# Kernel tuning notes

Hardware: AMD Instinct MI355X
Metric: run time of the kernel (lower is better)

Reference implementation:

```python
import jax, jax.numpy as jnp
import numpy as np

EMBED_DIM = 1024
NUM_HEADS = 16
HEAD_DIM = EMBED_DIM // NUM_HEADS
SCALING = HEAD_DIM ** -0.5
TGT_LEN, BSZ = 2048, 2


def setup_inputs() -> dict:
    key = jax.random.key(0)
    k1, k2, k3 = jax.random.split(key, 3)
    return {
        "query": jax.random.normal(k1, (TGT_LEN, BSZ, EMBED_DIM), jnp.float32),
        "in_proj_weight": jax.random.normal(k2, (3 * EMBED_DIM, EMBED_DIM), jnp.float32) * (EMBED_DIM ** -0.5),
        "in_proj_bias": jnp.zeros((3 * EMBED_DIM,), jnp.float32),
        "out_w": jax.random.normal(k3, (EMBED_DIM, EMBED_DIM), jnp.float32) * (EMBED_DIM ** -0.5),
        "out_b": jnp.zeros((EMBED_DIM,), jnp.float32),
    }


def reference(query, in_proj_weight, in_proj_bias, out_w, out_b):
    tgt_len, bsz, embed_dim = query.shape
    # fused QKV projection (self-attention path: qkv_same)
    qkv = query @ in_proj_weight.T + in_proj_bias  # [T, B, 3E]
    q, k, v = jnp.split(qkv, 3, axis=-1)
    q = q * SCALING
    # [T, B, E] -> [B*H, T, hd]
    def to_heads(x):
        return x.reshape(tgt_len, bsz * NUM_HEADS, HEAD_DIM).transpose(1, 0, 2)
    q, k, v = to_heads(q), to_heads(k), to_heads(v)
    attn_weights = jnp.einsum('bqd,bkd->bqk', q, k)          # [B*H, T, T]
    attn_weights = jax.nn.softmax(attn_weights, axis=-1)
    attn = jnp.einsum('bqk,bkd->bqd', attn_weights, v)       # [B*H, T, hd]
    attn = attn.transpose(1, 0, 2).reshape(tgt_len, bsz, embed_dim)
    attn = attn @ out_w.T + out_b
    # averaged attention weights over heads (need_weights=True)
    avg_weights = attn_weights.reshape(bsz, NUM_HEADS, tgt_len, tgt_len).mean(axis=1)
    return attn, avg_weights
```

## Files before the change

### kernel.cpp

```cpp
#include <hip/hip_runtime.h>
#include <hip/hip_bf16.h>
#include <math.h>

#define T_LEN 2048
#define BSZ   2
#define EMB   1024
#define NH    16
#define HD    64
#define BHN   (BSZ*NH)
#define M1    (T_LEN*BSZ)
#define SCAL  0.125f
#define QSCALE (0.125f * 1.44269504088896f)

typedef __attribute__((ext_vector_type(8))) short bf16x8;
typedef __attribute__((ext_vector_type(4))) float f32x4;
typedef __attribute__((ext_vector_type(2))) unsigned int u32x2;

__device__ inline unsigned short f2bf(float x) {
    union { float f; unsigned u; } v; v.f = x;
    unsigned r = v.u + 0x7FFF + ((v.u >> 16) & 1);
    return (unsigned short)(r >> 16);
}

__device__ inline unsigned pack2bf(float a, float b) {
    union { __hip_bfloat162 h; unsigned u; } v;
    v.h = __float22bfloat162_rn(make_float2(a, b));
    return v.u;
}

__device__ inline float fexp2(float x) {
#if __has_builtin(__builtin_amdgcn_exp2f)
    return __builtin_amdgcn_exp2f(x);
#else
    return exp2f(x);
#endif
}

__device__ inline void async16(const unsigned short* g, unsigned short* l) {
    __builtin_amdgcn_global_load_lds(
        (const __attribute__((address_space(1))) void*)g,
        (__attribute__((address_space(3))) void*)l, 16, 0, 0);
}

__device__ inline void hard_barrier() {
    __builtin_amdgcn_sched_barrier(0);
    asm volatile("" ::: "memory");
    __builtin_amdgcn_s_barrier();
    asm volatile("" ::: "memory");
    __builtin_amdgcn_sched_barrier(0);
}

__device__ inline unsigned short* swz(unsigned short* base, int r, int c) {
    return base + (((r << 3) + (c ^ (r & 7))) << 3);
}
__device__ inline const unsigned short* swz(const unsigned short* base, int r, int c) {
    return base + (((r << 3) + (c ^ (r & 7))) << 3);
}

__device__ inline void xchg(unsigned e, unsigned o, unsigned& w_lo, unsigned& w_hi) {
#if __has_builtin(__builtin_amdgcn_permlane32_swap) && __has_builtin(__builtin_amdgcn_permlane16_swap)
    u32x2 x = __builtin_amdgcn_permlane32_swap(e, o, false, false);
    u32x2 y = __builtin_amdgcn_permlane16_swap(x[0], x[1], false, false);
    w_lo = y[0]; w_hi = y[1];
#else
    int lane = (int)(threadIdx.x & 63);
    int quad = lane >> 4, l16 = lane & 15;
    int srcA = ((quad & 1) * 2) * 16 + l16;
    int srcB = ((quad & 1) * 2 + 1) * 16 + l16;
    unsigned ea = (unsigned)__shfl((int)e, srcA, 64);
    unsigned oa = (unsigned)__shfl((int)o, srcA, 64);
    unsigned eb = (unsigned)__shfl((int)e, srcB, 64);
    unsigned ob = (unsigned)__shfl((int)o, srcB, 64);
    w_lo = (quad >> 1) ? oa : ea;
    w_hi = (quad >> 1) ? ob : eb;
#endif
}

__global__ __launch_bounds__(256) void cvt3_kernel(
    const float* __restrict__ s0, const float* __restrict__ s1,
    const float* __restrict__ s2, unsigned short* __restrict__ dst,
    int n0, int n1)
{
    int idx = blockIdx.x * 256 + threadIdx.x;
    const float* src; int o;
    if (idx < n0)           { src = s0; o = idx; }
    else if (idx < n0 + n1) { src = s1; o = idx - n0; }
    else                    { src = s2; o = idx - n0 - n1; }
    float4 a = reinterpret_cast<const float4*>(src)[(size_t)o * 2];
    float4 c = reinterpret_cast<const float4*>(src)[(size_t)o * 2 + 1];
    unsigned w[4] = { pack2bf(a.x, a.y), pack2bf(a.z, a.w),
                      pack2bf(c.x, c.y), pack2bf(c.z, c.w) };
    reinterpret_cast<uint4*>(dst)[idx] = *reinterpret_cast<uint4*>(w);
}

__global__ __launch_bounds__(256) void qkv_mfma_kernel(
    const unsigned short* __restrict__ A, const unsigned short* __restrict__ B,
    const float* __restrict__ bias,
    unsigned short* __restrict__ Q16, unsigned short* __restrict__ K16,
    unsigned short* __restrict__ Vt16)
{
    constexpr int BM = 128, BN = 128, BK = 32, K = 1024;
    __shared__ unsigned short As[BM * BK];
    __shared__ unsigned short Bs[BN * BK];
    const int tid = threadIdx.x;
    const int lane = tid & 63, wave = tid >> 6;
    const int quad = lane >> 4, l16 = lane & 15;
    const int wr = wave >> 1, wc = wave & 1;
    const int m0 = blockIdx.x * BM, n0 = blockIdx.y * BN;

    f32x4 zero4 = {0.f, 0.f, 0.f, 0.f};
    f32x4 acc[4][4];
    #pragma unroll
    for (int i = 0; i < 4; ++i)
        #pragma unroll
        for (int j = 0; j < 4; ++j) acc[i][j] = zero4;

    for (int k0 = 0; k0 < K; k0 += BK) {
        __syncthreads();
        #pragma unroll
        for (int t = 0; t < 2; ++t) {
            int c = t * 256 + tid;
            int m = c >> 2, kb = c & 3;
            async16(&A[(size_t)(m0 + m) * K + k0 + kb * 8], &As[c * 8]);
            async16(&B[(size_t)(n0 + m) * K + k0 + kb * 8], &Bs[c * 8]);
        }
        __syncthreads();
        bf16x8 af[4], bfr[4];
        #pragma unroll
        for (int i = 0; i < 4; ++i) {
            af[i]  = *reinterpret_cast<const bf16x8*>(&As[(wr * 64 + i * 16 + l16) * BK + quad * 8]);
            bfr[i] = *reinterpret_cast<const bf16x8*>(&Bs[(wc * 64 + i * 16 + l16) * BK + quad * 8]);
        }
        #pragma unroll
        for (int i = 0; i < 4; ++i)
            #pragma unroll
            for (int j = 0; j < 4; ++j)
                acc[i][j] = __builtin_amdgcn_mfma_f32_16x16x32_bf16(af[i], bfr[j], acc[i][j], 0, 0, 0);
    }

    #pragma unroll
    for (int j = 0; j < 4; ++j) {
        int n = n0 + wc * 64 + j * 16 + l16;
        float bv = bias[n];
        int which = n >> 10;
        int c = n & 1023;
        int h = c >> 6, d = c & 63;
        #pragma unroll
        for (int i = 0; i < 4; ++i) {
            #pragma unroll
            for (int r = 0; r < 4; ++r) {
                int m = m0 + wr * 64 + i * 16 + quad * 4 + r;
                int t = m >> 1, b = m & 1;
                int bh = b * NH + h;
                float v = acc[i][j][r] + bv;
                if (which == 0)      Q16[((size_t)bh * T_LEN + t) * HD + d] = f2bf(v * QSCALE);
                else if (which == 1) K16[((size_t)bh * T_LEN + t) * HD + d] = f2bf(v);
                else                 Vt16[((size_t)bh * HD + d) * T_LEN + t] = f2bf(v);
            }
        }
    }
}

__global__ __launch_bounds__(256) void flash_mfma_kernel(
    const unsigned short* __restrict__ Qb, const unsigned short* __restrict__ Kb,
    const unsigned short* __restrict__ Vt, unsigned short* __restrict__ AO,
    float* __restrict__ Lrow)
{
    __shared__ unsigned short Ks[2][64 * 64];
    __shared__ unsigned short Vs[2][64 * 64];
    const int tid = threadIdx.x;
    const int lane = tid & 63, wave = tid >> 6;
    const int quad = lane >> 4, l16 = lane & 15;

    const int lin = blockIdx.y * gridDim.x + blockIdx.x;
    const int xcd = lin & 7, slot = lin >> 3;
    const int bh = xcd * 4 + (slot >> 5);
    const int qt = slot & 31;
    const int q0 = qt * 64;
    const int b = bh >> 4, h = bh & 15;

    const unsigned short* Qp = Qb + ((size_t)bh * T_LEN + q0 + wave * 16 + l16) * HD;
    bf16x8 qf0 = *reinterpret_cast<const bf16x8*>(Qp + quad * 8);
    bf16x8 qf1 = *reinterpret_cast<const bf16x8*>(Qp + 32 + quad * 8);

    f32x4 zero4 = {0.f, 0.f, 0.f, 0.f};
    f32x4 oacc[4] = {zero4, zero4, zero4, zero4};
    float l_i = 0.f;

    const unsigned short* Kbase = Kb + (size_t)bh * T_LEN * HD;
    const unsigned short* Vbase = Vt + (size_t)bh * HD * T_LEN;

    const int cl0 = tid, cl1 = tid + 256;
    const int r0 = cl0 >> 3, c0 = (cl0 & 7) ^ (r0 & 7);
    const int r1 = cl1 >> 3, c1 = (cl1 & 7) ^ (r1 & 7);

    async16(&Kbase[(size_t)r0 * HD + c0 * 8], &Ks[0][cl0 * 8]);
    async16(&Kbase[(size_t)r1 * HD + c1 * 8], &Ks[0][cl1 * 8]);
    async16(&Vbase[(size_t)r0 * T_LEN + c0 * 8], &Vs[0][cl0 * 8]);
    async16(&Vbase[(size_t)r1 * T_LEN + c1 * 8], &Vs[0][cl1 * 8]);

    int cur = 0;
    for (int kt = 0; kt < T_LEN; kt += 64) {
        if (kt + 64 < T_LEN) {
            const int nb = cur ^ 1, nkt = kt + 64;
            async16(&Kbase[(size_t)(nkt + r0) * HD + c0 * 8], &Ks[nb][cl0 * 8]);
            async16(&Kbase[(size_t)(nkt + r1) * HD + c1 * 8], &Ks[nb][cl1 * 8]);
            async16(&Vbase[(size_t)r0 * T_LEN + nkt + c0 * 8], &Vs[nb][cl0 * 8]);
            async16(&Vbase[(size_t)r1 * T_LEN + nkt + c1 * 8], &Vs[nb][cl1 * 8]);
            asm volatile("s_waitcnt vmcnt(4)" ::: "memory");
        } else {
            asm volatile("s_waitcnt vmcnt(0)" ::: "memory");
        }
        hard_barrier();

        const unsigned short* Kt = Ks[cur];
        const unsigned short* Vv = Vs[cur];

        f32x4 sacc[4] = {zero4, zero4, zero4, zero4};
        __builtin_amdgcn_s_setprio(1);
        #pragma unroll
        for (int kb = 0; kb < 4; ++kb) {
            bf16x8 kf0 = *reinterpret_cast<const bf16x8*>(swz(Kt, kb * 16 + l16, quad));
            sacc[kb] = __builtin_amdgcn_mfma_f32_16x16x32_bf16(kf0, qf0, sacc[kb], 0, 0, 0);
            bf16x8 kf1 = *reinterpret_cast<const bf16x8*>(swz(Kt, kb * 16 + l16, 4 + quad));
            sacc[kb] = __builtin_amdgcn_mfma_f32_16x16x32_bf16(kf1, qf1, sacc[kb], 0, 0, 0);
        }
        __builtin_amdgcn_s_setprio(0);

        float psum = 0.f;
        unsigned dlo[4], dhi[4];
        #pragma unroll
        for (int kb = 0; kb < 4; ++kb) {
            float p0 = fexp2(sacc[kb][0]);
            float p1 = fexp2(sacc[kb][1]);
            float p2 = fexp2(sacc[kb][2]);
            float p3 = fexp2(sacc[kb][3]);
            psum += (p0 + p1) + (p2 + p3);
            dlo[kb] = pack2bf(p0, p1);
            dhi[kb] = pack2bf(p2, p3);
        }
        psum += __shfl_xor(psum, 16);
        psum += __shfl_xor(psum, 32);
        l_i += psum;

        bf16x8 pfrag[2];
        #pragma unroll
        for (int s = 0; s < 2; ++s) {
            unsigned w0, w1, w2, w3;
            xchg(dlo[2 * s], dlo[2 * s + 1], w0, w2);
            xchg(dhi[2 * s], dhi[2 * s + 1], w1, w3);
            union { bf16x8 v; unsigned u[4]; } P;
            P.u[0] = w0; P.u[1] = w1; P.u[2] = w2; P.u[3] = w3;
            pfrag[s] = P.v;
        }

        __builtin_amdgcn_s_setprio(1);
        #pragma unroll
        for (int s = 0; s < 2; ++s) {
            #pragma unroll
            for (int dt = 0; dt < 4; ++dt) {
                bf16x8 va = *reinterpret_cast<const bf16x8*>(swz(Vv, dt * 16 + l16, s * 4 + quad));
                oacc[dt] = __builtin_amdgcn_mfma_f32_16x16x32_bf16(va, pfrag[s], oacc[dt], 0, 0, 0);
            }
        }
        __builtin_amdgcn_s_setprio(0);

        hard_barrier();
        cur ^= 1;
    }

    float rl = 1.0f / l_i;
    int q = q0 + wave * 16 + l16;
    size_t base = ((size_t)q * BSZ + b) * EMB + h * HD;
    #pragma unroll
    for (int dt = 0; dt < 4; ++dt) {
        unsigned o[2] = { pack2bf(oacc[dt][0] * rl, oacc[dt][1] * rl),
                          pack2bf(oacc[dt][2] * rl, oacc[dt][3] * rl) };
        *reinterpret_cast<uint2*>(&AO[base + dt * 16 + quad * 4]) = *reinterpret_cast<uint2*>(o);
    }
    if (quad == 0)
        Lrow[(size_t)bh * T_LEN + q] = l_i;
}

__global__ __launch_bounds__(256) void avg_mfma_kernel(
    const unsigned short* __restrict__ Qb, const unsigned short* __restrict__ Kb,
    const float* __restrict__ Lrow, float* __restrict__ avg_out)
{
    __shared__ unsigned short Ks[2][64 * 64];
    const int tid = threadIdx.x;
    const int lane = tid & 63, wave = tid >> 6;
    const int quad = lane >> 4, l16 = lane & 15;
    const int kt = blockIdx.x, qt = blockIdx.y, b = blockIdx.z;
    const int q0 = qt * 64, k0 = kt * 64;

    const int cl0 = tid, cl1 = tid + 256;
    const int r0 = cl0 >> 3, c0 = (cl0 & 7) ^ (r0 & 7);
    const int r1 = cl1 >> 3, c1 = (cl1 & 7) ^ (r1 & 7);

    f32x4 zero4 = {0.f, 0.f, 0.f, 0.f};
    f32x4 acc[4] = {zero4, zero4, zero4, zero4};

    {
        const unsigned short* Kg = Kb + ((size_t)(b * NH) * T_LEN + k0) * HD;
        async16(&Kg[(size_t)r0 * HD + c0 * 8], &Ks[0][cl0 * 8]);
        async16(&Kg[(size_t)r1 * HD + c1 * 8], &Ks[0][cl1 * 8]);
    }

    int cur = 0;
    for (int h = 0; h < NH; ++h) {
        int bh = b * NH + h;
        const unsigned short* Qp = Qb + ((size_t)bh * T_LEN + q0 + wave * 16 + l16) * HD;
        bf16x8 qf0 = *reinterpret_cast<const bf16x8*>(Qp + quad * 8);
        bf16x8 qf1 = *reinterpret_cast<const bf16x8*>(Qp + 32 + quad * 8);

        if (h + 1 < NH) {
            const unsigned short* Kg = Kb + ((size_t)(bh + 1) * T_LEN + k0) * HD;
            int nb = cur ^ 1;
            async16(&Kg[(size_t)r0 * HD + c0 * 8], &Ks[nb][cl0 * 8]);
            async16(&Kg[(size_t)r1 * HD + c1 * 8], &Ks[nb][cl1 * 8]);
            asm volatile("s_waitcnt vmcnt(4)" ::: "memory");
        } else {
            asm volatile("s_waitcnt vmcnt(2)" ::: "memory");
        }
        hard_barrier();

        f32x4 sacc[4] = {zero4, zero4, zero4, zero4};
        __builtin_amdgcn_s_setprio(1);
        #pragma unroll
        for (int c = 0; c < 4; ++c) {
            bf16x8 kb0 = *reinterpret_cast<const bf16x8*>(swz(Ks[cur], c * 16 + l16, quad));
            sacc[c] = __builtin_amdgcn_mfma_f32_16x16x32_bf16(qf0, kb0, sacc[c], 0, 0, 0);
            bf16x8 kb1 = *reinterpret_cast<const bf16x8*>(swz(Ks[cur], c * 16 + l16, 4 + quad));
            sacc[c] = __builtin_amdgcn_mfma_f32_16x16x32_bf16(qf1, kb1, sacc[c], 0, 0, 0);
        }
        __builtin_amdgcn_s_setprio(0);
        #pragma unroll
        for (int r = 0; r < 4; ++r) {
            int q = q0 + wave * 16 + quad * 4 + r;
            float rl = 1.0f / Lrow[(size_t)bh * T_LEN + q];
            #pragma unroll
            for (int c = 0; c < 4; ++c)
                acc[c][r] += fexp2(sacc[c][r]) * rl;
        }
        hard_barrier();
        cur ^= 1;
    }
    #pragma unroll
    for (int r = 0; r < 4; ++r) {
        int q = q0 + wave * 16 + quad * 4 + r;
        size_t base = ((size_t)b * T_LEN + q) * T_LEN + k0;
        #pragma unroll
        for (int c = 0; c < 4; ++c)
            avg_out[base + c * 16 + l16] = acc[c][r] * (1.0f / 16.0f);
    }
}

__global__ __launch_bounds__(256) void out_mfma_kernel(
    const unsigned short* __restrict__ A, const unsigned short* __restrict__ B,
    const float* __restrict__ bias, float* __restrict__ out)
{
    constexpr int BM = 128, BN = 128, BK = 32, K = 1024;
    __shared__ unsigned short As[BM * BK];
    __shared__ unsigned short Bs[BN * BK];
    const int tid = threadIdx.x;
    const int lane = tid & 63, wave = tid >> 6;
    const int quad = lane >> 4, l16 = lane & 15;
    const int wr = wave >> 1, wc = wave & 1;
    const int m0 = blockIdx.x * BM, n0 = blockIdx.y * BN;

    f32x4 zero4 = {0.f, 0.f, 0.f, 0.f};
    f32x4 acc[4][4];
    #pragma unroll
    for (int i = 0; i < 4; ++i)
        #pragma unroll
        for (int j = 0; j < 4; ++j) acc[i][j] = zero4;

    for (int k0 = 0; k0 < K; k0 += BK) {
        __syncthreads();
        #pragma unroll
        for (int t = 0; t < 2; ++t) {
            int c = t * 256 + tid;
            int m = c >> 2, kb = c & 3;
            async16(&A[(size_t)(m0 + m) * K + k0 + kb * 8], &As[c * 8]);
            async16(&B[(size_t)(n0 + m) * K + k0 + kb * 8], &Bs[c * 8]);
        }
        __syncthreads();
        bf16x8 af[4], bfr[4];
        #pragma unroll
        for (int i = 0; i < 4; ++i) {
            af[i]  = *reinterpret_cast<const bf16x8*>(&As[(wr * 64 + i * 16 + l16) * BK + quad * 8]);
            bfr[i] = *reinterpret_cast<const bf16x8*>(&Bs[(wc * 64 + i * 16 + l16) * BK + quad * 8]);
        }
        #pragma unroll
        for (int i = 0; i < 4; ++i)
            #pragma unroll
            for (int j = 0; j < 4; ++j)
                acc[i][j] = __builtin_amdgcn_mfma_f32_16x16x32_bf16(af[i], bfr[j], acc[i][j], 0, 0, 0);
    }

    #pragma unroll
    for (int j = 0; j < 4; ++j) {
        int n = n0 + wc * 64 + j * 16 + l16;
        float bv = bias[n];
        #pragma unroll
        for (int i = 0; i < 4; ++i) {
            #pragma unroll
            for (int r = 0; r < 4; ++r) {
                int m = m0 + wr * 64 + i * 16 + quad * 4 + r;
                out[(size_t)m * 1024 + n] = acc[i][j][r] + bv;
            }
        }
    }
}

extern "C" void kernel_launch(void* const* d_in, const int* in_sizes, int n_in,
                              void* d_out, int out_size, void* d_ws, size_t ws_size,
                              hipStream_t stream)
{
    const float* query = (const float*)d_in[0];
    const float* wqkv  = (const float*)d_in[1];
    const float* bqkv  = (const float*)d_in[2];
    const float* wout  = (const float*)d_in[3];
    const float* bout  = (const float*)d_in[4];
    float* out = (float*)d_out;

    char* ws = (char*)d_ws;
    const size_t E_Q   = (size_t)M1 * EMB;
    const size_t E_W   = (size_t)3 * EMB * EMB;
    const size_t E_WO  = (size_t)EMB * EMB;
    const size_t E_QKV = (size_t)BHN * T_LEN * HD;

    unsigned short* queryb = (unsigned short*)ws;
    unsigned short* wqkvb  = queryb + E_Q;
    unsigned short* woutb  = wqkvb + E_W;
    unsigned short* Q16    = woutb + E_WO;
    unsigned short* K16    = Q16 + E_QKV;
    unsigned short* Vt16   = K16 + E_QKV;
    unsigned short* AO16   = Vt16 + E_QKV;
    float* Lr = (float*)(AO16 + E_Q);
    const size_t need = (E_Q + E_W + E_WO + 4 * E_QKV) * 2 + (size_t)BHN * T_LEN * 4;
    if (ws_size < need) return;

    cvt3_kernel<<<(int)((E_Q + E_W + E_WO) / 8 / 256), 256, 0, stream>>>(
        query, wqkv, wout, queryb, (int)(E_Q / 8), (int)(E_W / 8));

    qkv_mfma_kernel<<<dim3(M1 / 128, 3072 / 128), 256, 0, stream>>>(queryb, wqkvb, bqkv, Q16, K16, Vt16);
    flash_mfma_kernel<<<dim3(T_LEN / 64, BHN), 256, 0, stream>>>(Q16, K16, Vt16, AO16, Lr);
    avg_mfma_kernel<<<dim3(T_LEN / 64, T_LEN / 64, BSZ), 256, 0, stream>>>(Q16, K16, Lr, out + (size_t)M1 * EMB);
    out_mfma_kernel<<<dim3(M1 / 128, 1024 / 128), 256, 0, stream>>>(AO16, woutb, bout, out);
}
```

Before: 259.9 us.

## Double avg-kernel query tile, stage K for two heads, store reciprocal row sums

The head-averaged attention-weight kernel now handles 128 query rows per block instead of 64. It loads K tiles for two heads per pipeline stage and keeps the K fragments in registers so they are reused across both query sub-tiles. The flash kernel now stores the reciprocal of the row sum, so the avg kernel reads it with one float4 load instead of doing per-row divides. The goal is fewer barriers, half as many K loads per output element, and fewer blocks, at the cost of more registers and LDS and possibly lower occupancy.

```diff
diff --git a/kernel.cpp b/kernel.cpp
--- a/kernel.cpp
+++ b/kernel.cpp
@@ -164,7 +164,7 @@
 __global__ __launch_bounds__(256) void flash_mfma_kernel(
     const unsigned short* __restrict__ Qb, const unsigned short* __restrict__ Kb,
     const unsigned short* __restrict__ Vt, unsigned short* __restrict__ AO,
-    float* __restrict__ Lrow)
+    float* __restrict__ Rrow)
 {
     __shared__ unsigned short Ks[2][64 * 64];
     __shared__ unsigned short Vs[2][64 * 64];
@@ -279,80 +279,100 @@
         *reinterpret_cast<uint2*>(&AO[base + dt * 16 + quad * 4]) = *reinterpret_cast<uint2*>(o);
     }
     if (quad == 0)
-        Lrow[(size_t)bh * T_LEN + q] = l_i;
+        Rrow[(size_t)bh * T_LEN + q] = rl;
 }
 
 __global__ __launch_bounds__(256) void avg_mfma_kernel(
     const unsigned short* __restrict__ Qb, const unsigned short* __restrict__ Kb,
-    const float* __restrict__ Lrow, float* __restrict__ avg_out)
-{
-    __shared__ unsigned short Ks[2][64 * 64];
+    const float* __restrict__ Rrow, float* __restrict__ avg_out)
+{
+    __shared__ unsigned short Ks[2][2][64 * 64];
     const int tid = threadIdx.x;
     const int lane = tid & 63, wave = tid >> 6;
     const int quad = lane >> 4, l16 = lane & 15;
     const int kt = blockIdx.x, qt = blockIdx.y, b = blockIdx.z;
-    const int q0 = qt * 64, k0 = kt * 64;
-
-    const int cl0 = tid, cl1 = tid + 256;
-    const int r0 = cl0 >> 3, c0 = (cl0 & 7) ^ (r0 & 7);
-    const int r1 = cl1 >> 3, c1 = (cl1 & 7) ^ (r1 & 7);
+    const int q0 = qt * 128, k0 = kt * 64;
+
+    auto stage_pair = [&](int buf, int h0) {
+        const unsigned short* Kg = Kb + ((size_t)(b * NH + h0) * T_LEN + k0) * HD;
+        #pragma unroll
+        for (int t = 0; t < 4; ++t) {
+            int c = t * 256 + tid;
+            int hh = c >> 9, cl = c & 511;
+            int r = cl >> 3, cc = (cl & 7) ^ (r & 7);
+            async16(&Kg[(size_t)hh * T_LEN * HD + (size_t)r * HD + cc * 8],
+                    &Ks[buf][0][0] + (size_t)c * 8);
+        }
+    };
 
     f32x4 zero4 = {0.f, 0.f, 0.f, 0.f};
-    f32x4 acc[4] = {zero4, zero4, zero4, zero4};
-
-    {
-        const unsigned short* Kg = Kb + ((size_t)(b * NH) * T_LEN + k0) * HD;
-        async16(&Kg[(size_t)r0 * HD + c0 * 8], &Ks[0][cl0 * 8]);
-        async16(&Kg[(size_t)r1 * HD + c1 * 8], &Ks[0][cl1 * 8]);
-    }
-
+    f32x4 acc[2][4];
+    #pragma unroll
+    for (int s = 0; s < 2; ++s)
+        #pragma unroll
+        for (int c = 0; c < 4; ++c) acc[s][c] = zero4;
+
+    stage_pair(0, 0);
     int cur = 0;
-    for (int h = 0; h < NH; ++h) {
-        int bh = b * NH + h;
-        const unsigned short* Qp = Qb + ((size_t)bh * T_LEN + q0 + wave * 16 + l16) * HD;
-        bf16x8 qf0 = *reinterpret_cast<const bf16x8*>(Qp + quad * 8);
-        bf16x8 qf1 = *reinterpret_cast<const bf16x8*>(Qp + 32 + quad * 8);
-
-        if (h + 1 < NH) {
-            const unsigned short* Kg = Kb + ((size_t)(bh + 1) * T_LEN + k0) * HD;
-            int nb = cur ^ 1;
-            async16(&Kg[(size_t)r0 * HD + c0 * 8], &Ks[nb][cl0 * 8]);
-            async16(&Kg[(size_t)r1 * HD + c1 * 8], &Ks[nb][cl1 * 8]);
+    for (int g = 0; g < NH / 2; ++g) {
+        if (g + 1 < NH / 2) {
+            stage_pair(cur ^ 1, 2 * (g + 1));
             asm volatile("s_waitcnt vmcnt(4)" ::: "memory");
         } else {
-            asm volatile("s_waitcnt vmcnt(2)" ::: "memory");
+            asm volatile("s_waitcnt vmcnt(0)" ::: "memory");
         }
         hard_barrier();
 
-        f32x4 sacc[4] = {zero4, zero4, zero4, zero4};
-        __builtin_amdgcn_s_setprio(1);
-        #pragma unroll
-        for (int c = 0; c < 4; ++c) {
-            bf16x8 kb0 = *reinterpret_cast<const bf16x8*>(swz(Ks[cur], c * 16 + l16, quad));
-            sacc[c] = __builtin_amdgcn_mfma_f32_16x16x32_bf16(qf0, kb0, sacc[c], 0, 0, 0);
-            bf16x8 kb1 = *reinterpret_cast<const bf16x8*>(swz(Ks[cur], c * 16 + l16, 4 + quad));
-            sacc[c] = __builtin_amdgcn_mfma_f32_16x16x32_bf16(qf1, kb1, sacc[c], 0, 0, 0);
-        }
-        __builtin_amdgcn_s_setprio(0);
-        #pragma unroll
-        for (int r = 0; r < 4; ++r) {
-            int q = q0 + wave * 16 + quad * 4 + r;
-            float rl = 1.0f / Lrow[(size_t)bh * T_LEN + q];
-            #pragma unroll
-            for (int c = 0; c < 4; ++c)
-                acc[c][r] += fexp2(sacc[c][r]) * rl;
+        #pragma unroll
+        for (int hh = 0; hh < 2; ++hh) {
+            const int bh = b * NH + 2 * g + hh;
+            const unsigned short* Kt = Ks[cur][hh];
+            bf16x8 kf[4][2];
+            #pragma unroll
+            for (int c = 0; c < 4; ++c) {
+                kf[c][0] = *reinterpret_cast<const bf16x8*>(swz(Kt, c * 16 + l16, quad));
+                kf[c][1] = *reinterpret_cast<const bf16x8*>(swz(Kt, c * 16 + l16, 4 + quad));
+            }
+            #pragma unroll
+            for (int s = 0; s < 2; ++s) {
+                const int qrow = q0 + s * 64 + wave * 16;
+                const unsigned short* Qp = Qb + ((size_t)bh * T_LEN + qrow + l16) * HD;
+                bf16x8 qf0 = *reinterpret_cast<const bf16x8*>(Qp + quad * 8);
+                bf16x8 qf1 = *reinterpret_cast<const bf16x8*>(Qp + 32 + quad * 8);
+                float4 rlv = *reinterpret_cast<const float4*>(
+                    &Rrow[(size_t)bh * T_LEN + qrow + quad * 4]);
+
+                f32x4 sacc[4] = {zero4, zero4, zero4, zero4};
+                __builtin_amdgcn_s_setprio(1);
+                #pragma unroll
+                for (int c = 0; c < 4; ++c) {
+                    sacc[c] = __builtin_amdgcn_mfma_f32_16x16x32_bf16(qf0, kf[c][0], sacc[c], 0, 0, 0);
+                    sacc[c] = __builtin_amdgcn_mfma_f32_16x16x32_bf16(qf1, kf[c][1], sacc[c], 0, 0, 0);
+                }
+                __builtin_amdgcn_s_setprio(0);
+
+                float rl4[4] = { rlv.x, rlv.y, rlv.z, rlv.w };
+                #pragma unroll
+                for (int c = 0; c < 4; ++c)
+                    #pragma unroll
+                    for (int r = 0; r < 4; ++r)
+                        acc[s][c][r] += fexp2(sacc[c][r]) * rl4[r];
+            }
         }
         hard_barrier();
         cur ^= 1;
     }
-    #pragma unroll
-    for (int r = 0; r < 4; ++r) {
-        int q = q0 + wave * 16 + quad * 4 + r;
-        size_t base = ((size_t)b * T_LEN + q) * T_LEN + k0;
-        #pragma unroll
-        for (int c = 0; c < 4; ++c)
-            avg_out[base + c * 16 + l16] = acc[c][r] * (1.0f / 16.0f);
-    }
+
+    #pragma unroll
+    for (int s = 0; s < 2; ++s)
+        #pragma unroll
+        for (int r = 0; r < 4; ++r) {
+            int q = q0 + s * 64 + wave * 16 + quad * 4 + r;
+            size_t base = ((size_t)b * T_LEN + q) * T_LEN + k0;
+            #pragma unroll
+            for (int c = 0; c < 4; ++c)
+                avg_out[base + c * 16 + l16] = acc[s][c][r] * (1.0f / 16.0f);
+        }
 }
 
 __global__ __launch_bounds__(256) void out_mfma_kernel(
@@ -446,6 +466,6 @@
 
     qkv_mfma_kernel<<<dim3(M1 / 128, 3072 / 128), 256, 0, stream>>>(queryb, wqkvb, bqkv, Q16, K16, Vt16);
     flash_mfma_kernel<<<dim3(T_LEN / 64, BHN), 256, 0, stream>>>(Q16, K16, Vt16, AO16, Lr);
-    avg_mfma_kernel<<<dim3(T_LEN / 64, T_LEN / 64, BSZ), 256, 0, stream>>>(Q16, K16, Lr, out + (size_t)M1 * EMB);
+    avg_mfma_kernel<<<dim3(T_LEN / 64, T_LEN / 128, BSZ), 256, 0, stream>>>(Q16, K16, Lr, out + (size_t)M1 * EMB);
     out_mfma_kernel<<<dim3(M1 / 128, 1024 / 128), 256, 0, stream>>>(AO16, woutb, bout, out);
 }
```

New measurement: 252.2 us. 3.0% less time.
